# Kernel tuning notes

Measured on AMD Instinct MI355X. Metric: run time of the kernel, lower is better.

The kernel has to match this reference:

```python
import jax, jax.numpy as jnp
import numpy as np

HID = 8
EMB = 32


def setup_inputs() -> dict:
    V = 32000
    S, B = 128, 32
    key = jax.random.key(0)
    ks = jax.random.split(key, 13)
    u = lambda k, shape, s: jax.random.uniform(k, shape, jnp.float32, -1.0 / np.sqrt(s), 1.0 / np.sqrt(s))
    return {
        "input_batch": jax.random.randint(ks[0], (S, B), 0, V, dtype=jnp.int64),
        "lookup": u(ks[1], (V, EMB), EMB),
        "weight_xf": u(ks[2], (EMB, HID), HID),
        "weight_hf": u(ks[3], (HID, HID), HID),
        "weight_xb": u(ks[4], (EMB, HID), HID),
        "weight_hb": u(ks[5], (HID, HID), HID),
        "weight_o": u(ks[6], (2 * HID, V), V),
        "Hf": u(ks[7], (HID,), HID),
        "Hb": u(ks[8], (HID,), HID),
        "bias_x": u(ks[9], (HID,), HID),
        "bias_hf": u(ks[10], (HID,), HID),
        "bias_hb": u(ks[11], (HID,), HID),
        "bias_o": u(ks[12], (V,), V),
    }


def reference(input_batch, lookup, weight_xf, weight_hf, weight_xb, weight_hb,
              weight_o, Hf, Hb, bias_x, bias_hf, bias_hb, bias_o):
    S, B = input_batch.shape
    X = lookup[input_batch]  # [S, B, EMB]

    # Forward Elman scan. Hf_table[i] = hidden BEFORE consuming x[i] (shifted).
    h0f = jnp.broadcast_to(Hf, (B, HID))

    def fstep(h, x):
        h2 = jnp.tanh(x @ weight_xf + bias_x + h @ weight_hf + bias_hf)
        return h2, h2

    _, hf = jax.lax.scan(fstep, h0f, X)
    Hf_table = jnp.concatenate([h0f[None], hf[:-1]], axis=0)  # [S, B, HID]

    # Backward Elman scan (reverse). hb[i] = hidden after consuming x[i..S-1];
    # original uses hidden after x[i+1..S-1] at position i (init at i=S-1).
    h0b = jnp.broadcast_to(Hb, (B, HID))

    def bstep(h, x):
        h2 = jnp.tanh(x @ weight_xb + bias_x + h @ weight_hb + bias_hb)
        return h2, h2

    _, hb = jax.lax.scan(bstep, h0b, X, reverse=True)
    Hb_table = jnp.concatenate([hb[1:], h0b[None]], axis=0)  # [S, B, HID]

    H = jnp.concatenate([Hf_table, Hb_table], axis=-1)  # [S, B, 2*HID]
    logits = H @ weight_o + bias_o  # [S, B, V]
    return jax.nn.log_softmax(logits, axis=-1)
```

## Files before the change

kernel.cpp:

```cpp
#include <hip/hip_runtime.h>
#include <hip/hip_bf16.h>

#define S_LEN 128
#define B_SZ  32
#define VOCAB 32000
#define EMB   32
#define HID   8
#define NROWS 4096

typedef float v2f __attribute__((ext_vector_type(2)));

#if defined(__has_builtin) && __has_builtin(__builtin_elementwise_fma)
__device__ __forceinline__ v2f fma2(v2f a, v2f b, v2f c) {
    return __builtin_elementwise_fma(a, b, c);
}
#else
__device__ __forceinline__ v2f fma2(v2f a, v2f b, v2f c) {
    v2f r; r.x = fmaf(a.x, b.x, c.x); r.y = fmaf(a.y, b.y, c.y); return r;
}
#endif

__global__ __launch_bounds__(256) void xproj_kernel(
        const int* __restrict__ idx,
        const float* __restrict__ lookup,
        const float* __restrict__ wxf,
        const float* __restrict__ wxb,
        const float* __restrict__ bias_x,
        const float* __restrict__ bias_hf,
        const float* __restrict__ bias_hb,
        float* __restrict__ xpF, float* __restrict__ xpB) {
    int tok = blockIdx.x * blockDim.x + threadIdx.x;
    if (tok >= NROWS) return;
    int e = idx[tok];
    const float* xr = lookup + (size_t)e * EMB;
    float x[EMB];
    #pragma unroll
    for (int i = 0; i < EMB; ++i) x[i] = xr[i];
    #pragma unroll
    for (int j = 0; j < HID; ++j) {
        float bx = bias_x[j];
        float fa = bx + bias_hf[j];
        float fb = bx + bias_hb[j];
        #pragma unroll
        for (int e2 = 0; e2 < EMB; ++e2) {
            float xv = x[e2];
            fa += xv * wxf[e2 * HID + j];
            fb += xv * wxb[e2 * HID + j];
        }
        xpF[(size_t)tok * HID + j] = fa;
        xpB[(size_t)tok * HID + j] = fb;
    }
}

__global__ __launch_bounds__(64) void scan_kernel(
        const float* __restrict__ xpF,
        const float* __restrict__ xpB,
        const float* __restrict__ whf,
        const float* __restrict__ whb,
        const float* __restrict__ Hf0,
        const float* __restrict__ Hb0,
        float* __restrict__ Hws) {
    int gtid = blockIdx.x * 64 + threadIdx.x;
    int j   = gtid & 7;
    int b   = (gtid >> 3) & 31;
    int dir = gtid >> 8;

    const float* wh = dir ? whb : whf;
    float w[HID];
    #pragma unroll
    for (int k = 0; k < HID; ++k) w[k] = wh[k * HID + j];

    const float* xp = dir ? xpB : xpF;
    float h = dir ? Hb0[j] : Hf0[j];

    int s0 = dir ? (S_LEN - 1) : 0;
    float xv = xp[(size_t)(s0 * B_SZ + b) * HID + j];

    for (int step = 0; step < S_LEN; ++step) {
        int s = dir ? (S_LEN - 1 - step) : step;
        int r = s * B_SZ + b;
        float xv_next = 0.0f;
        if (step + 1 < S_LEN) {
            int sn = dir ? (S_LEN - 2 - step) : (step + 1);
            xv_next = xp[(size_t)(sn * B_SZ + b) * HID + j];
        }
        Hws[(size_t)r * 16 + dir * HID + j] = h;
        float acc = xv;
        #pragma unroll
        for (int k = 0; k < HID; ++k)
            acc += __shfl(h, k, 8) * w[k];
        float ex = __expf(2.0f * acc);
        h = 1.0f - 2.0f * __builtin_amdgcn_rcpf(ex + 1.0f);
        xv = xv_next;
    }
}

__global__ __launch_bounds__(256) void repack_kernel(
        const float* __restrict__ wo, float* __restrict__ wo_p) {
    int v2 = blockIdx.x * blockDim.x + threadIdx.x;
    if (v2 >= VOCAB / 2) return;
    float2 buf[16];
    #pragma unroll
    for (int k = 0; k < 16; ++k)
        buf[k] = *reinterpret_cast<const float2*>(wo + (size_t)k * VOCAB + 2 * v2);
    float4* dst = reinterpret_cast<float4*>(wo_p + (size_t)v2 * 32);
    #pragma unroll
    for (int q = 0; q < 8; ++q)
        dst[q] = make_float4(buf[2 * q].x, buf[2 * q].y,
                             buf[2 * q + 1].x, buf[2 * q + 1].y);
}

#define VCH_A 256
#define NCH_A (VOCAB / VCH_A)
__global__ __launch_bounds__(256) void passA_kernel(
        const float* __restrict__ Hws,
        const float* __restrict__ wo_p,
        const float* __restrict__ bias_o,
        float* __restrict__ Zpart) {
    int r = blockIdx.y * 256 + threadIdx.x;
    int p0 = blockIdx.x * (VCH_A / 2);

    float h[16];
    const float4* hr4 = reinterpret_cast<const float4*>(Hws + (size_t)r * 16);
    #pragma unroll
    for (int q = 0; q < 4; ++q) {
        float4 f = hr4[q];
        h[4 * q + 0] = f.x; h[4 * q + 1] = f.y;
        h[4 * q + 2] = f.z; h[4 * q + 3] = f.w;
    }

    float z = 0.0f;
    #pragma unroll 2
    for (int p = 0; p < VCH_A / 2; ++p) {
        const v2f* wp = reinterpret_cast<const v2f*>(wo_p + (size_t)(p0 + p) * 32);
        float2 bb = *reinterpret_cast<const float2*>(bias_o + (size_t)(p0 + p) * 2);
        v2f acc; acc.x = bb.x; acc.y = bb.y;
        #pragma unroll
        for (int k = 0; k < 16; ++k) {
            v2f hk; hk.x = h[k]; hk.y = h[k];
            acc = fma2(hk, wp[k], acc);
        }
        z += __expf(acc.x) + __expf(acc.y);
    }
    Zpart[(size_t)blockIdx.x * NROWS + r] = z;
}

__global__ __launch_bounds__(256) void logz_kernel(
        const float* __restrict__ Zpart, float* __restrict__ logZ) {
    int r = blockIdx.x * blockDim.x + threadIdx.x;
    if (r >= NROWS) return;
    float s = 0.0f;
    for (int i = 0; i < NCH_A; ++i) s += Zpart[(size_t)i * NROWS + r];
    logZ[r] = logf(s);
}

#define MT_B 128
__global__ __launch_bounds__(256) void passB_kernel(
        const float* __restrict__ Hws,
        const float* __restrict__ wo,
        const float* __restrict__ bias_o,
        const float* __restrict__ logZ,
        float* __restrict__ out) {
    int t = threadIdx.x;
    int v = (blockIdx.x * 256 + t) * 4;
    if (v >= VOCAB) return;
    int r0 = blockIdx.y * MT_B;

    v2f w01[16], w23[16];
    #pragma unroll
    for (int k = 0; k < 16; ++k) {
        float4 w4 = *reinterpret_cast<const float4*>(wo + (size_t)k * VOCAB + v);
        w01[k].x = w4.x; w01[k].y = w4.y;
        w23[k].x = w4.z; w23[k].y = w4.w;
    }
    float4 bv = *reinterpret_cast<const float4*>(bias_o + v);
    v2f b01; b01.x = bv.x; b01.y = bv.y;
    v2f b23; b23.x = bv.z; b23.y = bv.w;

    #pragma unroll 2
    for (int rr = 0; rr < MT_B; ++rr) {
        int r = r0 + rr;
        const float* hr = Hws + (size_t)r * 16;
        v2f t01 = b01, t23 = b23;
        #pragma unroll
        for (int k = 0; k < 16; ++k) {
            float hk = hr[k];
            v2f hk2; hk2.x = hk; hk2.y = hk;
            t01 = fma2(hk2, w01[k], t01);
            t23 = fma2(hk2, w23[k], t23);
        }
        float lz = logZ[r];
        float4 o = make_float4(t01.x - lz, t01.y - lz, t23.x - lz, t23.y - lz);
        *reinterpret_cast<float4*>(out + (size_t)r * VOCAB + v) = o;
    }
}

extern "C" void kernel_launch(void* const* d_in, const int* in_sizes, int n_in,
                              void* d_out, int out_size, void* d_ws, size_t ws_size,
                              hipStream_t stream) {
    const int*   idx     = (const int*)d_in[0];
    const float* lookup  = (const float*)d_in[1];
    const float* wxf     = (const float*)d_in[2];
    const float* whf     = (const float*)d_in[3];
    const float* wxb     = (const float*)d_in[4];
    const float* whb     = (const float*)d_in[5];
    const float* wo      = (const float*)d_in[6];
    const float* Hf0     = (const float*)d_in[7];
    const float* Hb0     = (const float*)d_in[8];
    const float* bias_x  = (const float*)d_in[9];
    const float* bias_hf = (const float*)d_in[10];
    const float* bias_hb = (const float*)d_in[11];
    const float* bias_o  = (const float*)d_in[12];
    float* out = (float*)d_out;

    float* ws    = (float*)d_ws;
    float* xpF   = ws;
    float* xpB   = ws + 32768;
    float* Hws   = ws + 65536;
    float* wo_p  = ws + 131072;
    float* Zpart = ws + 643072;
    float* logZ  = ws + 1155072;

    xproj_kernel<<<16, 256, 0, stream>>>(idx, lookup, wxf, wxb,
                                         bias_x, bias_hf, bias_hb, xpF, xpB);
    scan_kernel<<<8, 64, 0, stream>>>(xpF, xpB, whf, whb, Hf0, Hb0, Hws);
    repack_kernel<<<63, 256, 0, stream>>>(wo, wo_p);
    passA_kernel<<<dim3(NCH_A, NROWS / 256), 256, 0, stream>>>(Hws, wo_p, bias_o, Zpart);
    logz_kernel<<<16, 256, 0, stream>>>(Zpart, logZ);
    passB_kernel<<<dim3(32, NROWS / MT_B), 256, 0, stream>>>(Hws, wo, bias_o, logZ, out);
}
```

Baseline: 681.9 us.

## Merge prep kernels, double rows per thread in passA, stage H in LDS for passB

Folds the x-projection and weight repack into one launch, which removes a kernel launch. passA now computes two rows per thread so each weight load is reused twice, halving the grid. passB stages the block's hidden rows and logZ in shared memory and writes the output with nontemporal stores, aiming to cut repeated global loads and cache pollution on the large 524 MB output write. The cost is higher register pressure in passA and an extra barrier in passB.

```diff
diff --git a/kernel.cpp b/kernel.cpp
--- a/kernel.cpp
+++ b/kernel.cpp
@@ -9,6 +9,7 @@
 #define NROWS 4096
 
 typedef float v2f __attribute__((ext_vector_type(2)));
+typedef float v4f __attribute__((ext_vector_type(4)));
 
 #if defined(__has_builtin) && __has_builtin(__builtin_elementwise_fma)
 __device__ __forceinline__ v2f fma2(v2f a, v2f b, v2f c) {
@@ -20,7 +21,7 @@
 }
 #endif
 
-__global__ __launch_bounds__(256) void xproj_kernel(
+__global__ __launch_bounds__(256) void prep_kernel(
         const int* __restrict__ idx,
         const float* __restrict__ lookup,
         const float* __restrict__ wxf,
@@ -28,27 +29,42 @@
         const float* __restrict__ bias_x,
         const float* __restrict__ bias_hf,
         const float* __restrict__ bias_hb,
-        float* __restrict__ xpF, float* __restrict__ xpB) {
-    int tok = blockIdx.x * blockDim.x + threadIdx.x;
-    if (tok >= NROWS) return;
-    int e = idx[tok];
-    const float* xr = lookup + (size_t)e * EMB;
-    float x[EMB];
-    #pragma unroll
-    for (int i = 0; i < EMB; ++i) x[i] = xr[i];
-    #pragma unroll
-    for (int j = 0; j < HID; ++j) {
-        float bx = bias_x[j];
-        float fa = bx + bias_hf[j];
-        float fb = bx + bias_hb[j];
-        #pragma unroll
-        for (int e2 = 0; e2 < EMB; ++e2) {
-            float xv = x[e2];
-            fa += xv * wxf[e2 * HID + j];
-            fb += xv * wxb[e2 * HID + j];
-        }
-        xpF[(size_t)tok * HID + j] = fa;
-        xpB[(size_t)tok * HID + j] = fb;
+        float* __restrict__ xpF, float* __restrict__ xpB,
+        const float* __restrict__ wo, float* __restrict__ wo_p) {
+    int blk = blockIdx.x;
+    if (blk < 16) {
+        int tok = blk * 256 + threadIdx.x;
+        int e = idx[tok];
+        const float* xr = lookup + (size_t)e * EMB;
+        float x[EMB];
+        #pragma unroll
+        for (int i = 0; i < EMB; ++i) x[i] = xr[i];
+        #pragma unroll
+        for (int j = 0; j < HID; ++j) {
+            float bx = bias_x[j];
+            float fa = bx + bias_hf[j];
+            float fb = bx + bias_hb[j];
+            #pragma unroll
+            for (int e2 = 0; e2 < EMB; ++e2) {
+                float xv = x[e2];
+                fa += xv * wxf[e2 * HID + j];
+                fb += xv * wxb[e2 * HID + j];
+            }
+            xpF[(size_t)tok * HID + j] = fa;
+            xpB[(size_t)tok * HID + j] = fb;
+        }
+    } else {
+        int v2 = (blk - 16) * 256 + threadIdx.x;
+        if (v2 >= VOCAB / 2) return;
+        float2 buf[16];
+        #pragma unroll
+        for (int k = 0; k < 16; ++k)
+            buf[k] = *reinterpret_cast<const float2*>(wo + (size_t)k * VOCAB + 2 * v2);
+        float4* dst = reinterpret_cast<float4*>(wo_p + (size_t)v2 * 32);
+        #pragma unroll
+        for (int q = 0; q < 8; ++q)
+            dst[q] = make_float4(buf[2 * q].x, buf[2 * q].y,
+                                 buf[2 * q + 1].x, buf[2 * q + 1].y);
     }
 }
 
@@ -95,21 +111,6 @@
     }
 }
 
-__global__ __launch_bounds__(256) void repack_kernel(
-        const float* __restrict__ wo, float* __restrict__ wo_p) {
-    int v2 = blockIdx.x * blockDim.x + threadIdx.x;
-    if (v2 >= VOCAB / 2) return;
-    float2 buf[16];
-    #pragma unroll
-    for (int k = 0; k < 16; ++k)
-        buf[k] = *reinterpret_cast<const float2*>(wo + (size_t)k * VOCAB + 2 * v2);
-    float4* dst = reinterpret_cast<float4*>(wo_p + (size_t)v2 * 32);
-    #pragma unroll
-    for (int q = 0; q < 8; ++q)
-        dst[q] = make_float4(buf[2 * q].x, buf[2 * q].y,
-                             buf[2 * q + 1].x, buf[2 * q + 1].y);
-}
-
 #define VCH_A 256
 #define NCH_A (VOCAB / VCH_A)
 __global__ __launch_bounds__(256) void passA_kernel(
@@ -117,32 +118,43 @@
         const float* __restrict__ wo_p,
         const float* __restrict__ bias_o,
         float* __restrict__ Zpart) {
-    int r = blockIdx.y * 256 + threadIdx.x;
+    int ra = blockIdx.y * 256 + threadIdx.x;
+    int rb = ra + (NROWS / 2);
     int p0 = blockIdx.x * (VCH_A / 2);
 
-    float h[16];
-    const float4* hr4 = reinterpret_cast<const float4*>(Hws + (size_t)r * 16);
+    float ha[16], hb[16];
+    const float4* ha4 = reinterpret_cast<const float4*>(Hws + (size_t)ra * 16);
+    const float4* hb4 = reinterpret_cast<const float4*>(Hws + (size_t)rb * 16);
     #pragma unroll
     for (int q = 0; q < 4; ++q) {
-        float4 f = hr4[q];
-        h[4 * q + 0] = f.x; h[4 * q + 1] = f.y;
-        h[4 * q + 2] = f.z; h[4 * q + 3] = f.w;
-    }
-
-    float z = 0.0f;
+        float4 fa = ha4[q];
+        float4 fb = hb4[q];
+        ha[4 * q + 0] = fa.x; ha[4 * q + 1] = fa.y;
+        ha[4 * q + 2] = fa.z; ha[4 * q + 3] = fa.w;
+        hb[4 * q + 0] = fb.x; hb[4 * q + 1] = fb.y;
+        hb[4 * q + 2] = fb.z; hb[4 * q + 3] = fb.w;
+    }
+
+    float za = 0.0f, zb = 0.0f;
     #pragma unroll 2
     for (int p = 0; p < VCH_A / 2; ++p) {
         const v2f* wp = reinterpret_cast<const v2f*>(wo_p + (size_t)(p0 + p) * 32);
         float2 bb = *reinterpret_cast<const float2*>(bias_o + (size_t)(p0 + p) * 2);
-        v2f acc; acc.x = bb.x; acc.y = bb.y;
+        v2f acca; acca.x = bb.x; acca.y = bb.y;
+        v2f accb = acca;
         #pragma unroll
         for (int k = 0; k < 16; ++k) {
-            v2f hk; hk.x = h[k]; hk.y = h[k];
-            acc = fma2(hk, wp[k], acc);
-        }
-        z += __expf(acc.x) + __expf(acc.y);
-    }
-    Zpart[(size_t)blockIdx.x * NROWS + r] = z;
+            v2f w = wp[k];
+            v2f hka; hka.x = ha[k]; hka.y = ha[k];
+            v2f hkb; hkb.x = hb[k]; hkb.y = hb[k];
+            acca = fma2(hka, w, acca);
+            accb = fma2(hkb, w, accb);
+        }
+        za += __expf(acca.x) + __expf(acca.y);
+        zb += __expf(accb.x) + __expf(accb.y);
+    }
+    Zpart[(size_t)blockIdx.x * NROWS + ra] = za;
+    Zpart[(size_t)blockIdx.x * NROWS + rb] = zb;
 }
 
 __global__ __launch_bounds__(256) void logz_kernel(
@@ -161,37 +173,51 @@
         const float* __restrict__ bias_o,
         const float* __restrict__ logZ,
         float* __restrict__ out) {
+    __shared__ __attribute__((aligned(16))) float hsh[MT_B * 16];
+    __shared__ float lz_sh[MT_B];
     int t = threadIdx.x;
+    int r0 = blockIdx.y * MT_B;
+
+    {
+        const float4* src = reinterpret_cast<const float4*>(Hws + (size_t)r0 * 16);
+        float4* dst = reinterpret_cast<float4*>(hsh);
+        dst[t]       = src[t];
+        dst[t + 256] = src[t + 256];
+        if (t < MT_B) lz_sh[t] = logZ[r0 + t];
+    }
+    __syncthreads();
+
     int v = (blockIdx.x * 256 + t) * 4;
-    if (v >= VOCAB) return;
-    int r0 = blockIdx.y * MT_B;
-
-    v2f w01[16], w23[16];
-    #pragma unroll
-    for (int k = 0; k < 16; ++k) {
-        float4 w4 = *reinterpret_cast<const float4*>(wo + (size_t)k * VOCAB + v);
-        w01[k].x = w4.x; w01[k].y = w4.y;
-        w23[k].x = w4.z; w23[k].y = w4.w;
-    }
-    float4 bv = *reinterpret_cast<const float4*>(bias_o + v);
-    v2f b01; b01.x = bv.x; b01.y = bv.y;
-    v2f b23; b23.x = bv.z; b23.y = bv.w;
-
-    #pragma unroll 2
-    for (int rr = 0; rr < MT_B; ++rr) {
-        int r = r0 + rr;
-        const float* hr = Hws + (size_t)r * 16;
-        v2f t01 = b01, t23 = b23;
+    if (v < VOCAB) {
+        v2f w01[16], w23[16];
         #pragma unroll
         for (int k = 0; k < 16; ++k) {
-            float hk = hr[k];
-            v2f hk2; hk2.x = hk; hk2.y = hk;
-            t01 = fma2(hk2, w01[k], t01);
-            t23 = fma2(hk2, w23[k], t23);
-        }
-        float lz = logZ[r];
-        float4 o = make_float4(t01.x - lz, t01.y - lz, t23.x - lz, t23.y - lz);
-        *reinterpret_cast<float4*>(out + (size_t)r * VOCAB + v) = o;
+            float4 w4 = *reinterpret_cast<const float4*>(wo + (size_t)k * VOCAB + v);
+            w01[k].x = w4.x; w01[k].y = w4.y;
+            w23[k].x = w4.z; w23[k].y = w4.w;
+        }
+        float4 bv = *reinterpret_cast<const float4*>(bias_o + v);
+        v2f b01; b01.x = bv.x; b01.y = bv.y;
+        v2f b23; b23.x = bv.z; b23.y = bv.w;
+
+        #pragma unroll 2
+        for (int rr = 0; rr < MT_B; ++rr) {
+            const float* hr = hsh + rr * 16;
+            v2f t01 = b01, t23 = b23;
+            #pragma unroll
+            for (int k = 0; k < 16; ++k) {
+                float hk = hr[k];
+                v2f hk2; hk2.x = hk; hk2.y = hk;
+                t01 = fma2(hk2, w01[k], t01);
+                t23 = fma2(hk2, w23[k], t23);
+            }
+            float lz = lz_sh[rr];
+            v4f o;
+            o.x = t01.x - lz; o.y = t01.y - lz;
+            o.z = t23.x - lz; o.w = t23.y - lz;
+            __builtin_nontemporal_store(
+                o, reinterpret_cast<v4f*>(out + (size_t)(r0 + rr) * VOCAB + v));
+        }
     }
 }
 
@@ -221,11 +247,11 @@
     float* Zpart = ws + 643072;
     float* logZ  = ws + 1155072;
 
-    xproj_kernel<<<16, 256, 0, stream>>>(idx, lookup, wxf, wxb,
-                                         bias_x, bias_hf, bias_hb, xpF, xpB);
+    prep_kernel<<<79, 256, 0, stream>>>(idx, lookup, wxf, wxb,
+                                        bias_x, bias_hf, bias_hb,
+                                        xpF, xpB, wo, wo_p);
     scan_kernel<<<8, 64, 0, stream>>>(xpF, xpB, whf, whb, Hf0, Hb0, Hws);
-    repack_kernel<<<63, 256, 0, stream>>>(wo, wo_p);
-    passA_kernel<<<dim3(NCH_A, NROWS / 256), 256, 0, stream>>>(Hws, wo_p, bias_o, Zpart);
+    passA_kernel<<<dim3(NCH_A, 8), 256, 0, stream>>>(Hws, wo_p, bias_o, Zpart);
     logz_kernel<<<16, 256, 0, stream>>>(Zpart, logZ);
     passB_kernel<<<dim3(32, NROWS / MT_B), 256, 0, stream>>>(Hws, wo, bias_o, logZ, out);
 }
```

Result: faster. 659.3 us (-3.3%).
